# Optimization experiments

Measured on AMD Instinct MI355X. Metric: run time of the kernel, lower is better.

Reference implementation:

```python
import jax, jax.numpy as jnp
import numpy as np

N_ATOMS = 4096
N_NEIGH = 32
IN_F = 128
HID = 256
OUT_F = 128
N_SPECIES = 64


def setup_inputs() -> dict:
    key = jax.random.key(0)
    k1, k2, k3, k4, k5, k6 = jax.random.split(key, 6)
    # kaiming-uniform-ish init scales (exact init doesn't matter for correctness testing)
    s1 = 1.0 / np.sqrt(IN_F)
    s2 = 1.0 / np.sqrt(HID)
    return {
        "features": jax.random.normal(k1, (N_ATOMS, N_NEIGH, IN_F), dtype=jnp.float32),
        "species_idx": jax.random.randint(k2, (N_ATOMS,), 0, N_SPECIES, dtype=jnp.int64 if jax.config.jax_enable_x64 else jnp.int32),
        "W1": jax.random.uniform(k3, (N_SPECIES, HID, IN_F), jnp.float32, -s1, s1),
        "b1": jax.random.uniform(k4, (N_SPECIES, HID), jnp.float32, -s1, s1),
        "W2": jax.random.uniform(k5, (N_SPECIES, OUT_F, HID), jnp.float32, -s2, s2),
        "b2": jax.random.uniform(k6, (N_SPECIES, OUT_F), jnp.float32, -s2, s2),
    }


def reference(features, species_idx, W1, b1, W2, b2):
    # Per-atom species-conditioned 2-layer MLP with SiLU after the hidden layer.
    # features: (A, N, in); W[idx]: (A, out, in) gathered per atom (as in torch W[idx]).
    x = jnp.einsum("ani,ahi->anh", features, W1[species_idx]) + b1[species_idx][:, None, :]
    x = jax.nn.silu(x)
    x = jnp.einsum("anh,aoh->ano", x, W2[species_idx]) + b2[species_idx][:, None, :]
    return x  # (A, N, out)
```

## Files before the change

### kernel.cpp

```cpp
#include <hip/hip_runtime.h>

typedef __attribute__((ext_vector_type(8))) short short8;
typedef __attribute__((ext_vector_type(4))) float f32x4;

#define N_ATOMS 4096
#define N_NEIGH 32
#define IN_F 128
#define HID 256
#define OUT_F 128
#define N_SPECIES 64

__device__ __forceinline__ unsigned short f2bf(float f) {
  unsigned u = __float_as_uint(f);
  u += 0x7FFF + ((u >> 16) & 1);
  return (unsigned short)(u >> 16);
}
struct HL { short h, l; };
__device__ __forceinline__ HL split2(float v) {
  unsigned u = __float_as_uint(v);
  float lo = v - __uint_as_float(u & 0xFFFF0000u);
  HL o;
  o.h = (short)(u >> 16);
  o.l = (short)(__float_as_uint(lo) >> 16);
  return o;
}

__global__ __launch_bounds__(256) void prep_kernel(
    const float* __restrict__ W1, const float* __restrict__ W2,
    const int* __restrict__ sp_idx,
    unsigned short* __restrict__ w1h, unsigned short* __restrict__ w2h,
    int* __restrict__ atom_order, int* __restrict__ sp_off, int* __restrict__ sp_cnt) {
  const int t = threadIdx.x;
  if (blockIdx.x == 0) {
    __shared__ int cnt[N_SPECIES], off[N_SPECIES], cur[N_SPECIES];
    if (t < N_SPECIES) cnt[t] = 0;
    __syncthreads();
    for (int a = t; a < N_ATOMS; a += 256) atomicAdd(&cnt[sp_idx[a]], 1);
    __syncthreads();
    if (t == 0) {
      int o = 0;
      for (int s = 0; s < N_SPECIES; ++s) { off[s] = o; cur[s] = o; o += cnt[s]; }
    }
    __syncthreads();
    for (int a = t; a < N_ATOMS; a += 256) {
      int s = sp_idx[a];
      atom_order[atomicAdd(&cur[s], 1)] = a;
    }
    if (t < N_SPECIES) { sp_off[t] = off[t]; sp_cnt[t] = cnt[t]; }
    return;
  }
  const int NV = (N_SPECIES * HID * IN_F) / 4;
  const int nsplit = (gridDim.x - 1) * 256;
  for (int v = (blockIdx.x - 1) * 256 + t; v < 2 * NV; v += nsplit) {
    const float4* src; unsigned short* dh; int j;
    if (v < NV) { src = (const float4*)W1; dh = w1h; j = v; }
    else        { src = (const float4*)W2; dh = w2h; j = v - NV; }
    float4 f = src[j];
    ushort4 h;
    h.x = f2bf(f.x); h.y = f2bf(f.y); h.z = f2bf(f.z); h.w = f2bf(f.w);
    ((ushort4*)dh)[j] = h;
  }
}

__global__ __launch_bounds__(512, 2) void mlp_kernel(
    const float* __restrict__ feat,
    const float* __restrict__ b1g, const float* __restrict__ b2g,
    const unsigned short* __restrict__ w1h, const unsigned short* __restrict__ w2h,
    const int* __restrict__ atom_order, const int* __restrict__ sp_off,
    const int* __restrict__ sp_cnt,
    float* __restrict__ out) {
  extern __shared__ char smem[];
  char* LW1 = smem;
  char* LW2 = smem + 65536;

  const int bid = blockIdx.x;
  const int s = (bid & 7) * 8 + (bid >> 5);
  const int p = (bid >> 3) & 3;
  const int tid = threadIdx.x;
  const int wave = tid >> 6, lane = tid & 63;
  const int q = lane >> 4, r = lane & 15;

  {
    const char* gw1 = (const char*)w1h + (long)s * (HID * IN_F * 2);
    const char* gw2 = (const char*)w2h + (long)s * (OUT_F * HID * 2);
#pragma unroll
    for (int it = 0; it < 8; ++it) {
      const int d = it * 8192 + tid * 16;
      const int pos = d >> 8, wb = d & 255;
      const int pl = pos & 31;
      const int hl = ((pl >> 2) & 3) * 8 + ((pl >> 4) & 1) * 4 + (pl & 3);
      const int srow = (pos & ~31) + hl;
      const int src = srow * (IN_F * 2) + (wb ^ ((pos & 7) << 4));
      __builtin_amdgcn_global_load_lds(
          (const __attribute__((address_space(1))) unsigned int*)(gw1 + src),
          (__attribute__((address_space(3))) unsigned int*)(LW1 + d), 16, 0, 0);
    }
#pragma unroll
    for (int it = 0; it < 8; ++it) {
      const int d = it * 8192 + tid * 16;
      const int o = d >> 9, wb = d & 511;
      const int src = o * (HID * 2) + (wb ^ ((o & 7) << 4));
      __builtin_amdgcn_global_load_lds(
          (const __attribute__((address_space(1))) unsigned int*)(gw2 + src),
          (__attribute__((address_space(3))) unsigned int*)(LW2 + d), 16, 0, 0);
    }
  }

  const int c = sp_cnt[s], base = sp_off[s];
  const int begin = base + (p * c) / 4;
  const int end   = base + ((p + 1) * c) / 4;

  const float* b1s = b1g + s * HID;
  const float* b2s = b2g + s * OUT_F;
  char* slab = smem + 131072 + wave * 4096;
  const int swz = (r & 7) << 4;

  asm volatile("s_waitcnt vmcnt(0)" ::: "memory");
  __syncthreads();

  for (int idx = begin + wave; idx < end; idx += 8) {
    const int atom = atom_order[idx];

    short8 fh[2][4], fl[2][4];
    {
      const float* fb = feat + (long)atom * (N_NEIGH * IN_F);
#pragma unroll
      for (int nt = 0; nt < 2; ++nt)
#pragma unroll
        for (int ks = 0; ks < 4; ++ks) {
          const float* ptr = fb + (16 * nt + r) * IN_F + 32 * ks + 8 * q;
          float4 v0 = *(const float4*)ptr;
          float4 v1 = *(const float4*)(ptr + 4);
          float vv[8] = {v0.x, v0.y, v0.z, v0.w, v1.x, v1.y, v1.z, v1.w};
          short8 h8, l8;
#pragma unroll
          for (int j = 0; j < 8; ++j) {
            HL hl = split2(vv[j]);
            h8[j] = hl.h;
            l8[j] = hl.l;
          }
          fh[nt][ks] = h8;
          fl[nt][ks] = l8;
        }
    }

    f32x4 oacc[8][2] = {};

    for (int hc = 0; hc < 8; ++hc) {
      f32x4 xacc[2][2] = {};
#pragma unroll
      for (int ks = 0; ks < 4; ++ks) {
        const int ib = ((32 * ks + 8 * q) * 2) ^ swz;
#pragma unroll
        for (int ht = 0; ht < 2; ++ht) {
          const int pos = 32 * hc + 16 * ht + r;
          short8 aw = *(const short8*)(LW1 + pos * 256 + ib);
          xacc[ht][0] = __builtin_amdgcn_mfma_f32_16x16x32_bf16(aw, fh[0][ks], xacc[ht][0], 0, 0, 0);
          xacc[ht][1] = __builtin_amdgcn_mfma_f32_16x16x32_bf16(aw, fh[1][ks], xacc[ht][1], 0, 0, 0);
          xacc[ht][0] = __builtin_amdgcn_mfma_f32_16x16x32_bf16(aw, fl[0][ks], xacc[ht][0], 0, 0, 0);
          xacc[ht][1] = __builtin_amdgcn_mfma_f32_16x16x32_bf16(aw, fl[1][ks], xacc[ht][1], 0, 0, 0);
        }
      }
      short8 xh[2], xl[2];
#pragma unroll
      for (int ht = 0; ht < 2; ++ht) {
        const float4 b1c = *(const float4*)(b1s + hc * 32 + 8 * q + 4 * ht);
        const float bb[4] = {b1c.x, b1c.y, b1c.z, b1c.w};
#pragma unroll
        for (int nt = 0; nt < 2; ++nt)
#pragma unroll
          for (int reg = 0; reg < 4; ++reg) {
            float v = xacc[ht][nt][reg] + bb[reg];
            v = v * __builtin_amdgcn_rcpf(1.0f + __expf(-v));
            HL hl = split2(v);
            xh[nt][4 * ht + reg] = hl.h;
            xl[nt][4 * ht + reg] = hl.l;
          }
      }
      const int kb = ((32 * hc + 8 * q) * 2) ^ swz;
#pragma unroll
      for (int ot = 0; ot < 8; ++ot) {
        const int row = 16 * ot + r;
        short8 aw = *(const short8*)(LW2 + row * 512 + kb);
        oacc[ot][0] = __builtin_amdgcn_mfma_f32_16x16x32_bf16(aw, xh[0], oacc[ot][0], 0, 0, 0);
        oacc[ot][1] = __builtin_amdgcn_mfma_f32_16x16x32_bf16(aw, xh[1], oacc[ot][1], 0, 0, 0);
        oacc[ot][0] = __builtin_amdgcn_mfma_f32_16x16x32_bf16(aw, xl[0], oacc[ot][0], 0, 0, 0);
        oacc[ot][1] = __builtin_amdgcn_mfma_f32_16x16x32_bf16(aw, xl[1], oacc[ot][1], 0, 0, 0);
      }
    }

    float* ob = out + (long)atom * (N_NEIGH * OUT_F);
#pragma unroll
    for (int g = 0; g < 4; ++g) {
#pragma unroll
      for (int oh = 0; oh < 2; ++oh) {
        const int ot = 2 * g + oh;
        const float4 b2c = *(const float4*)(b2s + 16 * ot + 4 * q);
        const float bb[4] = {b2c.x, b2c.y, b2c.z, b2c.w};
#pragma unroll
        for (int nt = 0; nt < 2; ++nt) {
          f32x4 v;
#pragma unroll
          for (int reg = 0; reg < 4; ++reg) v[reg] = oacc[ot][nt][reg] + bb[reg];
          const int n = 16 * nt + r;
          const int byte = n * 128 + (((16 * oh + 4 * q) * 4) ^ ((n & 7) << 4));
          *(f32x4*)(slab + byte) = v;
        }
      }
      __builtin_amdgcn_s_waitcnt(0);
#pragma unroll
      for (int m = 0; m < 4; ++m) {
        const int n = m * 8 + (lane >> 3);
        const int cb = ((lane & 7) * 16) ^ ((n & 7) << 4);
        float4 v = *(const float4*)(slab + n * 128 + cb);
        *(float4*)(ob + n * OUT_F + 32 * g + (lane & 7) * 4) = v;
      }
      __builtin_amdgcn_s_waitcnt(0);
    }
  }
}

extern "C" void kernel_launch(void* const* d_in, const int* in_sizes, int n_in,
                              void* d_out, int out_size, void* d_ws, size_t ws_size,
                              hipStream_t stream) {
  const float* feat = (const float*)d_in[0];
  const int* sp     = (const int*)d_in[1];
  const float* W1   = (const float*)d_in[2];
  const float* b1   = (const float*)d_in[3];
  const float* W2   = (const float*)d_in[4];
  const float* b2   = (const float*)d_in[5];
  float* out = (float*)d_out;

  char* ws = (char*)d_ws;
  unsigned short* w1h = (unsigned short*)(ws + 0);
  unsigned short* w2h = (unsigned short*)(ws + 4194304);
  int* atom_order = (int*)(ws + 8388608);
  int* sp_off     = (int*)(ws + 8388608 + 16384);
  int* sp_cnt     = (int*)(ws + 8388608 + 16384 + 256);

  hipFuncSetAttribute((const void*)mlp_kernel,
                      hipFuncAttributeMaxDynamicSharedMemorySize, 163840);

  hipLaunchKernelGGL(prep_kernel, dim3(1025), dim3(256), 0, stream,
                     W1, W2, sp, w1h, w2h, atom_order, sp_off, sp_cnt);
  hipLaunchKernelGGL(mlp_kernel, dim3(256), dim3(512), 163840, stream,
                     feat, b1, b2, w1h, w2h, atom_order, sp_off, sp_cnt, out);
}
```

Before: 181.4 us.

## Read species weights directly from global memory, one atom per wave

Drops the per-block LDS staging of a whole species' W1/W2 (128 KB) and the per-species block partitioning. Each wave now handles one atom from the species-sorted order, with 512 blocks of 8 waves, and reads bf16 weight fragments straight from global or L2. The row permutation that used to be applied during LDS staging moves into the prep kernel. This removes the large LDS fill and per-species load imbalance and raises occupancy, at the cost of repeated global/L2 weight reads inside the MFMA loops.

```diff
diff --git a/kernel.cpp b/kernel.cpp
--- a/kernel.cpp
+++ b/kernel.cpp
@@ -28,195 +28,168 @@
 __global__ __launch_bounds__(256) void prep_kernel(
     const float* __restrict__ W1, const float* __restrict__ W2,
     const int* __restrict__ sp_idx,
-    unsigned short* __restrict__ w1h, unsigned short* __restrict__ w2h,
-    int* __restrict__ atom_order, int* __restrict__ sp_off, int* __restrict__ sp_cnt) {
+    unsigned short* __restrict__ w1p, unsigned short* __restrict__ w2h,
+    int* __restrict__ atom_order) {
   const int t = threadIdx.x;
   if (blockIdx.x == 0) {
-    __shared__ int cnt[N_SPECIES], off[N_SPECIES], cur[N_SPECIES];
+    __shared__ int cnt[N_SPECIES], cur[N_SPECIES];
     if (t < N_SPECIES) cnt[t] = 0;
     __syncthreads();
     for (int a = t; a < N_ATOMS; a += 256) atomicAdd(&cnt[sp_idx[a]], 1);
     __syncthreads();
     if (t == 0) {
       int o = 0;
-      for (int s = 0; s < N_SPECIES; ++s) { off[s] = o; cur[s] = o; o += cnt[s]; }
+      for (int s = 0; s < N_SPECIES; ++s) { cur[s] = o; o += cnt[s]; }
     }
     __syncthreads();
     for (int a = t; a < N_ATOMS; a += 256) {
       int s = sp_idx[a];
       atom_order[atomicAdd(&cur[s], 1)] = a;
     }
-    if (t < N_SPECIES) { sp_off[t] = off[t]; sp_cnt[t] = cnt[t]; }
     return;
   }
   const int NV = (N_SPECIES * HID * IN_F) / 4;
   const int nsplit = (gridDim.x - 1) * 256;
   for (int v = (blockIdx.x - 1) * 256 + t; v < 2 * NV; v += nsplit) {
-    const float4* src; unsigned short* dh; int j;
-    if (v < NV) { src = (const float4*)W1; dh = w1h; j = v; }
-    else        { src = (const float4*)W2; dh = w2h; j = v - NV; }
-    float4 f = src[j];
+    float4 f;
+    unsigned short* dst;
+    int j;
+    if (v < NV) {
+      j = v;
+      const int s0 = j >> 13;
+      const int rem = j & 8191;
+      const int drow = rem >> 5;
+      const int c4 = rem & 31;
+      const int pl = drow & 31;
+      const int srow = (drow & ~31) + ((pl >> 2) & 3) * 8 + ((pl >> 4) & 1) * 4 + (pl & 3);
+      f = ((const float4*)W1)[(s0 * HID + srow) * (IN_F / 4) + c4];
+      dst = w1p;
+    } else {
+      j = v - NV;
+      f = ((const float4*)W2)[j];
+      dst = w2h;
+    }
     ushort4 h;
     h.x = f2bf(f.x); h.y = f2bf(f.y); h.z = f2bf(f.z); h.w = f2bf(f.w);
-    ((ushort4*)dh)[j] = h;
+    ((ushort4*)dst)[j] = h;
   }
 }
 
 __global__ __launch_bounds__(512, 2) void mlp_kernel(
     const float* __restrict__ feat,
     const float* __restrict__ b1g, const float* __restrict__ b2g,
-    const unsigned short* __restrict__ w1h, const unsigned short* __restrict__ w2h,
-    const int* __restrict__ atom_order, const int* __restrict__ sp_off,
-    const int* __restrict__ sp_cnt,
+    const unsigned short* __restrict__ w1p, const unsigned short* __restrict__ w2h,
+    const int* __restrict__ atom_order, const int* __restrict__ sp_idx,
     float* __restrict__ out) {
-  extern __shared__ char smem[];
-  char* LW1 = smem;
-  char* LW2 = smem + 65536;
+  __shared__ char smem[8][4096];
 
   const int bid = blockIdx.x;
-  const int s = (bid & 7) * 8 + (bid >> 5);
-  const int p = (bid >> 3) & 3;
-  const int tid = threadIdx.x;
-  const int wave = tid >> 6, lane = tid & 63;
+  const int orig = (bid & 7) * 64 + (bid >> 3);
+  const int wave = threadIdx.x >> 6, lane = threadIdx.x & 63;
   const int q = lane >> 4, r = lane & 15;
 
-  {
-    const char* gw1 = (const char*)w1h + (long)s * (HID * IN_F * 2);
-    const char* gw2 = (const char*)w2h + (long)s * (OUT_F * HID * 2);
-#pragma unroll
-    for (int it = 0; it < 8; ++it) {
-      const int d = it * 8192 + tid * 16;
-      const int pos = d >> 8, wb = d & 255;
-      const int pl = pos & 31;
-      const int hl = ((pl >> 2) & 3) * 8 + ((pl >> 4) & 1) * 4 + (pl & 3);
-      const int srow = (pos & ~31) + hl;
-      const int src = srow * (IN_F * 2) + (wb ^ ((pos & 7) << 4));
-      __builtin_amdgcn_global_load_lds(
-          (const __attribute__((address_space(1))) unsigned int*)(gw1 + src),
-          (__attribute__((address_space(3))) unsigned int*)(LW1 + d), 16, 0, 0);
-    }
-#pragma unroll
-    for (int it = 0; it < 8; ++it) {
-      const int d = it * 8192 + tid * 16;
-      const int o = d >> 9, wb = d & 511;
-      const int src = o * (HID * 2) + (wb ^ ((o & 7) << 4));
-      __builtin_amdgcn_global_load_lds(
-          (const __attribute__((address_space(1))) unsigned int*)(gw2 + src),
-          (__attribute__((address_space(3))) unsigned int*)(LW2 + d), 16, 0, 0);
-    }
-  }
-
-  const int c = sp_cnt[s], base = sp_off[s];
-  const int begin = base + (p * c) / 4;
-  const int end   = base + ((p + 1) * c) / 4;
-
+  const int atom = atom_order[orig * 8 + wave];
+  const int s = sp_idx[atom];
+  const char* gw1 = (const char*)w1p + (long)s * (HID * IN_F * 2);
+  const char* gw2 = (const char*)w2h + (long)s * (OUT_F * HID * 2);
   const float* b1s = b1g + s * HID;
   const float* b2s = b2g + s * OUT_F;
-  char* slab = smem + 131072 + wave * 4096;
-  const int swz = (r & 7) << 4;
-
-  asm volatile("s_waitcnt vmcnt(0)" ::: "memory");
-  __syncthreads();
-
-  for (int idx = begin + wave; idx < end; idx += 8) {
-    const int atom = atom_order[idx];
-
-    short8 fh[2][4], fl[2][4];
-    {
-      const float* fb = feat + (long)atom * (N_NEIGH * IN_F);
+  char* slab = smem[wave];
+
+  short8 fh[2][4], fl[2][4];
+  {
+    const float* fb = feat + (long)atom * (N_NEIGH * IN_F);
+#pragma unroll
+    for (int nt = 0; nt < 2; ++nt)
+#pragma unroll
+      for (int ks = 0; ks < 4; ++ks) {
+        const float* ptr = fb + (16 * nt + r) * IN_F + 32 * ks + 8 * q;
+        float4 v0 = *(const float4*)ptr;
+        float4 v1 = *(const float4*)(ptr + 4);
+        float vv[8] = {v0.x, v0.y, v0.z, v0.w, v1.x, v1.y, v1.z, v1.w};
+        short8 h8, l8;
+#pragma unroll
+        for (int j = 0; j < 8; ++j) {
+          HL hl = split2(vv[j]);
+          h8[j] = hl.h;
+          l8[j] = hl.l;
+        }
+        fh[nt][ks] = h8;
+        fl[nt][ks] = l8;
+      }
+  }
+
+  f32x4 oacc[8][2] = {};
+
+  for (int hc = 0; hc < 8; ++hc) {
+    f32x4 xacc[2][2] = {};
+#pragma unroll
+    for (int ks = 0; ks < 4; ++ks) {
+      const int ib = (32 * ks + 8 * q) * 2;
+#pragma unroll
+      for (int ht = 0; ht < 2; ++ht) {
+        const int pos = 32 * hc + 16 * ht + r;
+        short8 aw = *(const short8*)(gw1 + pos * 256 + ib);
+        xacc[ht][0] = __builtin_amdgcn_mfma_f32_16x16x32_bf16(aw, fh[0][ks], xacc[ht][0], 0, 0, 0);
+        xacc[ht][1] = __builtin_amdgcn_mfma_f32_16x16x32_bf16(aw, fh[1][ks], xacc[ht][1], 0, 0, 0);
+        xacc[ht][0] = __builtin_amdgcn_mfma_f32_16x16x32_bf16(aw, fl[0][ks], xacc[ht][0], 0, 0, 0);
+        xacc[ht][1] = __builtin_amdgcn_mfma_f32_16x16x32_bf16(aw, fl[1][ks], xacc[ht][1], 0, 0, 0);
+      }
+    }
+    short8 xh[2], xl[2];
+#pragma unroll
+    for (int ht = 0; ht < 2; ++ht) {
+      const float4 b1c = *(const float4*)(b1s + hc * 32 + 8 * q + 4 * ht);
+      const float bb[4] = {b1c.x, b1c.y, b1c.z, b1c.w};
 #pragma unroll
       for (int nt = 0; nt < 2; ++nt)
 #pragma unroll
-        for (int ks = 0; ks < 4; ++ks) {
-          const float* ptr = fb + (16 * nt + r) * IN_F + 32 * ks + 8 * q;
-          float4 v0 = *(const float4*)ptr;
-          float4 v1 = *(const float4*)(ptr + 4);
-          float vv[8] = {v0.x, v0.y, v0.z, v0.w, v1.x, v1.y, v1.z, v1.w};
-          short8 h8, l8;
-#pragma unroll
-          for (int j = 0; j < 8; ++j) {
-            HL hl = split2(vv[j]);
-            h8[j] = hl.h;
-            l8[j] = hl.l;
-          }
-          fh[nt][ks] = h8;
-          fl[nt][ks] = l8;
+        for (int reg = 0; reg < 4; ++reg) {
+          float v = xacc[ht][nt][reg] + bb[reg];
+          v = v * __builtin_amdgcn_rcpf(1.0f + __expf(-v));
+          HL hl = split2(v);
+          xh[nt][4 * ht + reg] = hl.h;
+          xl[nt][4 * ht + reg] = hl.l;
         }
     }
-
-    f32x4 oacc[8][2] = {};
-
-    for (int hc = 0; hc < 8; ++hc) {
-      f32x4 xacc[2][2] = {};
-#pragma unroll
-      for (int ks = 0; ks < 4; ++ks) {
-        const int ib = ((32 * ks + 8 * q) * 2) ^ swz;
-#pragma unroll
-        for (int ht = 0; ht < 2; ++ht) {
-          const int pos = 32 * hc + 16 * ht + r;
-          short8 aw = *(const short8*)(LW1 + pos * 256 + ib);
-          xacc[ht][0] = __builtin_amdgcn_mfma_f32_16x16x32_bf16(aw, fh[0][ks], xacc[ht][0], 0, 0, 0);
-          xacc[ht][1] = __builtin_amdgcn_mfma_f32_16x16x32_bf16(aw, fh[1][ks], xacc[ht][1], 0, 0, 0);
-          xacc[ht][0] = __builtin_amdgcn_mfma_f32_16x16x32_bf16(aw, fl[0][ks], xacc[ht][0], 0, 0, 0);
-          xacc[ht][1] = __builtin_amdgcn_mfma_f32_16x16x32_bf16(aw, fl[1][ks], xacc[ht][1], 0, 0, 0);
-        }
+    const int kb = 64 * hc + 16 * q;
+#pragma unroll
+    for (int ot = 0; ot < 8; ++ot) {
+      short8 aw = *(const short8*)(gw2 + (16 * ot + r) * 512 + kb);
+      oacc[ot][0] = __builtin_amdgcn_mfma_f32_16x16x32_bf16(aw, xh[0], oacc[ot][0], 0, 0, 0);
+      oacc[ot][1] = __builtin_amdgcn_mfma_f32_16x16x32_bf16(aw, xh[1], oacc[ot][1], 0, 0, 0);
+      oacc[ot][0] = __builtin_amdgcn_mfma_f32_16x16x32_bf16(aw, xl[0], oacc[ot][0], 0, 0, 0);
+      oacc[ot][1] = __builtin_amdgcn_mfma_f32_16x16x32_bf16(aw, xl[1], oacc[ot][1], 0, 0, 0);
+    }
+  }
+
+  float* ob = out + (long)atom * (N_NEIGH * OUT_F);
+#pragma unroll
+  for (int g = 0; g < 4; ++g) {
+#pragma unroll
+    for (int oh = 0; oh < 2; ++oh) {
+      const int ot = 2 * g + oh;
+      const float4 b2c = *(const float4*)(b2s + 16 * ot + 4 * q);
+      const float bb[4] = {b2c.x, b2c.y, b2c.z, b2c.w};
+#pragma unroll
+      for (int nt = 0; nt < 2; ++nt) {
+        f32x4 v;
+#pragma unroll
+        for (int reg = 0; reg < 4; ++reg) v[reg] = oacc[ot][nt][reg] + bb[reg];
+        const int n = 16 * nt + r;
+        const int byte = n * 128 + (((16 * oh + 4 * q) * 4) ^ ((n & 7) << 4));
+        *(f32x4*)(slab + byte) = v;
       }
-      short8 xh[2], xl[2];
-#pragma unroll
-      for (int ht = 0; ht < 2; ++ht) {
-        const float4 b1c = *(const float4*)(b1s + hc * 32 + 8 * q + 4 * ht);
-        const float bb[4] = {b1c.x, b1c.y, b1c.z, b1c.w};
-#pragma unroll
-        for (int nt = 0; nt < 2; ++nt)
-#pragma unroll
-          for (int reg = 0; reg < 4; ++reg) {
-            float v = xacc[ht][nt][reg] + bb[reg];
-            v = v * __builtin_amdgcn_rcpf(1.0f + __expf(-v));
-            HL hl = split2(v);
-            xh[nt][4 * ht + reg] = hl.h;
-            xl[nt][4 * ht + reg] = hl.l;
-          }
-      }
-      const int kb = ((32 * hc + 8 * q) * 2) ^ swz;
-#pragma unroll
-      for (int ot = 0; ot < 8; ++ot) {
-        const int row = 16 * ot + r;
-        short8 aw = *(const short8*)(LW2 + row * 512 + kb);
-        oacc[ot][0] = __builtin_amdgcn_mfma_f32_16x16x32_bf16(aw, xh[0], oacc[ot][0], 0, 0, 0);
-        oacc[ot][1] = __builtin_amdgcn_mfma_f32_16x16x32_bf16(aw, xh[1], oacc[ot][1], 0, 0, 0);
-        oacc[ot][0] = __builtin_amdgcn_mfma_f32_16x16x32_bf16(aw, xl[0], oacc[ot][0], 0, 0, 0);
-        oacc[ot][1] = __builtin_amdgcn_mfma_f32_16x16x32_bf16(aw, xl[1], oacc[ot][1], 0, 0, 0);
-      }
-    }
-
-    float* ob = out + (long)atom * (N_NEIGH * OUT_F);
-#pragma unroll
-    for (int g = 0; g < 4; ++g) {
-#pragma unroll
-      for (int oh = 0; oh < 2; ++oh) {
-        const int ot = 2 * g + oh;
-        const float4 b2c = *(const float4*)(b2s + 16 * ot + 4 * q);
-        const float bb[4] = {b2c.x, b2c.y, b2c.z, b2c.w};
-#pragma unroll
-        for (int nt = 0; nt < 2; ++nt) {
-          f32x4 v;
-#pragma unroll
-          for (int reg = 0; reg < 4; ++reg) v[reg] = oacc[ot][nt][reg] + bb[reg];
-          const int n = 16 * nt + r;
-          const int byte = n * 128 + (((16 * oh + 4 * q) * 4) ^ ((n & 7) << 4));
-          *(f32x4*)(slab + byte) = v;
-        }
-      }
-      __builtin_amdgcn_s_waitcnt(0);
-#pragma unroll
-      for (int m = 0; m < 4; ++m) {
-        const int n = m * 8 + (lane >> 3);
-        const int cb = ((lane & 7) * 16) ^ ((n & 7) << 4);
-        float4 v = *(const float4*)(slab + n * 128 + cb);
-        *(float4*)(ob + n * OUT_F + 32 * g + (lane & 7) * 4) = v;
-      }
-      __builtin_amdgcn_s_waitcnt(0);
-    }
+    }
+    __builtin_amdgcn_s_waitcnt(0);
+#pragma unroll
+    for (int m = 0; m < 4; ++m) {
+      const int n = m * 8 + (lane >> 3);
+      const int cb = ((lane & 7) * 16) ^ ((n & 7) << 4);
+      float4 v = *(const float4*)(slab + n * 128 + cb);
+      *(float4*)(ob + n * OUT_F + 32 * g + (lane & 7) * 4) = v;
+    }
+    __builtin_amdgcn_s_waitcnt(0);
   }
 }
 
@@ -232,17 +205,12 @@
   float* out = (float*)d_out;
 
   char* ws = (char*)d_ws;
-  unsigned short* w1h = (unsigned short*)(ws + 0);
+  unsigned short* w1p = (unsigned short*)(ws + 0);
   unsigned short* w2h = (unsigned short*)(ws + 4194304);
   int* atom_order = (int*)(ws + 8388608);
-  int* sp_off     = (int*)(ws + 8388608 + 16384);
-  int* sp_cnt     = (int*)(ws + 8388608 + 16384 + 256);
-
-  hipFuncSetAttribute((const void*)mlp_kernel,
-                      hipFuncAttributeMaxDynamicSharedMemorySize, 163840);
 
   hipLaunchKernelGGL(prep_kernel, dim3(1025), dim3(256), 0, stream,
-                     W1, W2, sp, w1h, w2h, atom_order, sp_off, sp_cnt);
-  hipLaunchKernelGGL(mlp_kernel, dim3(256), dim3(512), 163840, stream,
-                     feat, b1, b2, w1h, w2h, atom_order, sp_off, sp_cnt, out);
-}
+                     W1, W2, sp, w1p, w2h, atom_order);
+  hipLaunchKernelGGL(mlp_kernel, dim3(512), dim3(512), 0, stream,
+                     feat, b1, b2, w1p, w2h, atom_order, sp, out);
+}
```

New measurement: 208.9 us. 1.15x slower.
